# Kernel optimization log

Hardware: AMD Instinct MI355X
Metric: run time of the kernel (lower is better)

Reference implementation:

```python
import jax, jax.numpy as jnp
import numpy as np

D_MODEL = 1024
N_HEADS = 16
D_K = D_MODEL // N_HEADS
THETA = 10000.0
MAX_SEQ_LEN = 2048


def _rope_tables(seq_len):
    pos = jnp.arange(seq_len, dtype=jnp.float32)
    inv_freq = 1.0 / (THETA ** (jnp.arange(0, D_K, 2, dtype=jnp.float32) / D_K))
    ang = pos[:, None] * inv_freq[None, :]  # [T, D_K/2]
    return jnp.cos(ang), jnp.sin(ang)


def _apply_rope(x, cos, sin):
    # x: [..., T, D_K]; cos/sin: [T, D_K/2]
    x_even = x[..., ::2]
    x_odd = x[..., 1::2]
    r_even = x_even * cos - x_odd * sin
    r_odd = x_even * sin + x_odd * cos
    out = jnp.stack([r_even, r_odd], axis=-1)  # [..., T, D_K/2, 2]
    return out.reshape(x.shape)


def setup_inputs() -> dict:
    key = jax.random.key(0)
    ks = jax.random.split(key, 5)
    std = np.sqrt(2.0 / (D_MODEL + D_MODEL))
    x = jax.random.normal(ks[0], (2, 2048, D_MODEL), dtype=jnp.float32)
    w_q = jax.random.normal(ks[1], (D_MODEL, D_MODEL), dtype=jnp.float32) * std
    w_k = jax.random.normal(ks[2], (D_MODEL, D_MODEL), dtype=jnp.float32) * std
    w_v = jax.random.normal(ks[3], (D_MODEL, D_MODEL), dtype=jnp.float32) * std
    w_o = jax.random.normal(ks[4], (D_MODEL, D_MODEL), dtype=jnp.float32) * std
    return {"x": x, "w_q": w_q, "w_k": w_k, "w_v": w_v, "w_o": w_o}


def reference(x, w_q, w_k, w_v, w_o):
    B, T, _ = x.shape
    # projections: weight stored as [d_out, d_in], y = x @ W^T
    q = jnp.einsum('btd,od->bto', x, w_q)
    k = jnp.einsum('btd,od->bto', x, w_k)
    v = jnp.einsum('btd,od->bto', x, w_v)
    # split heads: [B, T, H*Dk] -> [B, H, T, Dk]
    q = q.reshape(B, T, N_HEADS, D_K).transpose(0, 2, 1, 3)
    k = k.reshape(B, T, N_HEADS, D_K).transpose(0, 2, 1, 3)
    v = v.reshape(B, T, N_HEADS, D_K).transpose(0, 2, 1, 3)
    cos, sin = _rope_tables(T)
    q = _apply_rope(q, cos, sin)
    k = _apply_rope(k, cos, sin)
    scores = jnp.einsum('bhqd,bhkd->bhqk', q, k) / np.sqrt(D_K).astype(np.float32)
    causal = jnp.tril(jnp.ones((T, T), dtype=bool))
    scores = jnp.where(causal, scores, -jnp.inf)
    attn = jax.nn.softmax(scores, axis=-1)
    out = jnp.einsum('bhqk,bhkd->bhqd', attn, v)
    out = out.transpose(0, 2, 1, 3).reshape(B, T, D_MODEL)
    return jnp.einsum('btd,od->bto', out, w_o)
```

## Files before the change

kernel.cpp:

```cpp
#include <hip/hip_runtime.h>
#include <hip/hip_bf16.h>

typedef __bf16 bf16_t;
typedef __bf16 bf16x8 __attribute__((ext_vector_type(8)));
typedef float f32x4 __attribute__((ext_vector_type(4)));
typedef short short4v __attribute__((ext_vector_type(4)));

#define D_MODEL 1024
#define T_SEQ 2048
#define NH 16
#define DKD 64
#define X_ELEMS (4194304u)
#define W_ELEMS (1048576u)

__device__ __forceinline__ void async16(const bf16_t* g, bf16_t* l) {
    __builtin_amdgcn_global_load_lds((const __attribute__((address_space(1))) void*)g,
                                     (__attribute__((address_space(3))) void*)l, 16, 0, 0);
}

__global__ __launch_bounds__(256) void convert_kernel(
    const float* __restrict__ x, const float* __restrict__ wq,
    const float* __restrict__ wk, const float* __restrict__ wv,
    const float* __restrict__ wo,
    bf16_t* __restrict__ xb, bf16_t* __restrict__ wqb, bf16_t* __restrict__ wkb,
    bf16_t* __restrict__ wvb, bf16_t* __restrict__ wob)
{
    size_t idx = ((size_t)blockIdx.x * 256 + threadIdx.x) * 4;
    const float* src; bf16_t* dst; size_t off;
    if (idx < X_ELEMS) { src = x; dst = xb; off = idx; }
    else {
        size_t r = idx - X_ELEMS;
        unsigned w = (unsigned)(r >> 20);
        off = r & (W_ELEMS - 1);
        src = (w == 0) ? wq : (w == 1) ? wk : (w == 2) ? wv : wo;
        dst = (w == 0) ? wqb : (w == 1) ? wkb : (w == 2) ? wvb : wob;
    }
    float4 v = *(const float4*)(src + off);
    union { bf16_t b[4]; short4v s; } u;
    u.b[0] = (bf16_t)v.x; u.b[1] = (bf16_t)v.y;
    u.b[2] = (bf16_t)v.z; u.b[3] = (bf16_t)v.w;
    *(short4v*)(dst + off) = u.s;
}

__global__ __launch_bounds__(256) void rope_kernel(float* __restrict__ cost, float* __restrict__ sint)
{
    int idx = blockIdx.x * 256 + threadIdx.x;
    int t = idx >> 5, i = idx & 31;
    float inv = expf(-0.28782313662425572f * (float)i);
    float ang = (float)t * inv;
    float s, c;
    sincosf(ang, &s, &c);
    cost[idx] = c; sint[idx] = s;
}

__global__ __launch_bounds__(256) void gemm_fused(
    const bf16_t* __restrict__ A,
    const bf16_t* __restrict__ W0, const bf16_t* __restrict__ W1, const bf16_t* __restrict__ W2,
    bf16_t* __restrict__ qout, bf16_t* __restrict__ kout, bf16_t* __restrict__ vout,
    const float* __restrict__ cost, const float* __restrict__ sint,
    float* __restrict__ fout, int modeBase)
{
    const int K = 1024;
    __shared__ bf16_t As[128 * 32];
    __shared__ bf16_t Bs[128 * 32];
    const int tid = threadIdx.x;
    const int wave = tid >> 6, lane = tid & 63;
    const int quad = lane >> 4, l16 = lane & 15;
    const int m0 = blockIdx.x * 128;
    const int n0 = blockIdx.y * 128;
    const int wm = (wave >> 1) * 64, wn = (wave & 1) * 64;
    const int mode = modeBase + blockIdx.z;
    const bf16_t* W = (mode == 1) ? W1 : (mode == 2) ? W2 : W0;

    const bf16_t* Afrag = (mode == 2) ? Bs : As;
    const bf16_t* Bfrag = (mode == 2) ? As : Bs;
    const int aoff = (mode == 2) ? wn : wm;
    const int boff = (mode == 2) ? wm : wn;

    const f32x4 fzero = {0.f, 0.f, 0.f, 0.f};
    f32x4 acc[4][4];
    #pragma unroll
    for (int i = 0; i < 4; ++i)
        #pragma unroll
        for (int j = 0; j < 4; ++j) acc[i][j] = fzero;

    for (int k0 = 0; k0 < K; k0 += 32) {
        __syncthreads();
        #pragma unroll
        for (int c = 0; c < 2; ++c) {
            int G = c * 256 + tid;
            int row = G >> 2, go = G & 3;
            async16(A + (size_t)(m0 + row) * K + (k0 + go * 8), As + (size_t)(c * 256 + wave * 64) * 8);
            async16(W + (size_t)(n0 + row) * K + (k0 + go * 8), Bs + (size_t)(c * 256 + wave * 64) * 8);
        }
        __syncthreads();
        bf16x8 af[4], bfv[4];
        #pragma unroll
        for (int mi = 0; mi < 4; ++mi)
            af[mi] = *(const bf16x8*)(Afrag + (aoff + mi * 16 + l16) * 32 + quad * 8);
        #pragma unroll
        for (int ni = 0; ni < 4; ++ni)
            bfv[ni] = *(const bf16x8*)(Bfrag + (boff + ni * 16 + l16) * 32 + quad * 8);
        #pragma unroll
        for (int mi = 0; mi < 4; ++mi)
            #pragma unroll
            for (int ni = 0; ni < 4; ++ni)
                acc[mi][ni] = __builtin_amdgcn_mfma_f32_16x16x32_bf16(af[mi], bfv[ni], acc[mi][ni], 0, 0, 0);
    }

    #pragma unroll
    for (int mi = 0; mi < 4; ++mi) {
        #pragma unroll
        for (int ni = 0; ni < 4; ++ni) {
            #pragma unroll
            for (int reg = 0; reg < 4; ++reg) {
                float v = acc[mi][ni][reg];
                if (mode == 2) {
                    int f   = n0 + wn + mi * 16 + quad * 4 + reg;
                    int tok = m0 + wm + ni * 16 + l16;
                    int t = tok & (T_SEQ - 1), b = tok >> 11;
                    int h = f >> 6, dk = f & 63;
                    vout[(((size_t)b * NH + h) * DKD + dk) * T_SEQ + t] = (bf16_t)v;
                } else {
                    int row = m0 + wm + mi * 16 + quad * 4 + reg;
                    int col = n0 + wn + ni * 16 + l16;
                    if (mode == 3) {
                        fout[(size_t)row * D_MODEL + col] = v;
                    } else {
                        int t = row & (T_SEQ - 1), b = row >> 11;
                        int h = col >> 6, dk = col & 63;
                        float vp = __shfl_xor(v, 1);
                        int fi = dk >> 1;
                        float c = cost[t * 32 + fi], s = sint[t * 32 + fi];
                        float r = (dk & 1) ? (vp * s + v * c) : (v * c - vp * s);
                        bf16_t* dst = (mode == 0) ? qout : kout;
                        dst[(((size_t)b * NH + h) * T_SEQ + t) * DKD + dk] = (bf16_t)r;
                    }
                }
            }
        }
    }
}

__global__ __launch_bounds__(256, 2) void attn_kernel(
    const bf16_t* __restrict__ Q, const bf16_t* __restrict__ Kb,
    const bf16_t* __restrict__ Vt, bf16_t* __restrict__ O)
{
    __shared__ bf16_t Ks[2][64 * 64];
    __shared__ bf16_t Vs[2][64 * 64];
    __shared__ bf16_t Pw[4][16 * 72];
    const int tid = threadIdx.x;
    const int wave = tid >> 6, lane = tid & 63;
    const int quad = lane >> 4, l16 = lane & 15;
    const int qb = (int)(gridDim.x - 1) - (int)blockIdx.x;
    const int bh = blockIdx.y;
    const int qw = qb * 128 + wave * 32;

    const bf16_t* kbase = Kb + (size_t)bh * T_SEQ * DKD;
    const bf16_t* vbase = Vt + (size_t)bh * DKD * T_SEQ;

    bf16x8 qf[2][2];
    #pragma unroll
    for (int j = 0; j < 2; ++j) {
        const bf16_t* qp = Q + ((size_t)bh * T_SEQ + qw + j * 16 + l16) * DKD;
        qf[j][0] = *(const bf16x8*)(qp + quad * 8);
        qf[j][1] = *(const bf16x8*)(qp + 32 + quad * 8);
    }
    const f32x4 fzero = {0.f, 0.f, 0.f, 0.f};
    f32x4 oacc[2][4];
    #pragma unroll
    for (int j = 0; j < 2; ++j)
        #pragma unroll
        for (int i = 0; i < 4; ++i) oacc[j][i] = fzero;
    float mrun[2] = {-__builtin_inff(), -__builtin_inff()};
    float lrun[2] = {0.f, 0.f};

    bf16_t* pw = &Pw[wave][0];
    const int nkt = 2 * qb + 2;

    auto stage = [&](int kt, int buf) {
        const int k0 = kt * 64;
        #pragma unroll
        for (int c = 0; c < 2; ++c) {
            int G = c * 256 + tid;
            int row = G >> 3, p = G & 7;
            int go = p ^ (row & 7);
            async16(kbase + (size_t)(k0 + row) * DKD + go * 8,
                    &Ks[buf][0] + (size_t)(c * 256 + wave * 64) * 8);
            async16(vbase + (size_t)row * T_SEQ + k0 + go * 8,
                    &Vs[buf][0] + (size_t)(c * 256 + wave * 64) * 8);
        }
    };

    stage(0, 0);
    for (int kt = 0; kt < nkt; ++kt) {
        __syncthreads();
        if (kt + 1 < nkt) stage(kt + 1, (kt + 1) & 1);
        const int k0 = kt * 64;
        if (k0 > qw + 31) continue;
        const bf16_t* Kc = &Ks[kt & 1][0];
        const bf16_t* Vc = &Vs[kt & 1][0];

        bf16x8 kf[4][2], vf[4][2];
        #pragma unroll
        for (int fi = 0; fi < 4; ++fi) {
            int r = fi * 16 + l16;
            #pragma unroll
            for (int ks = 0; ks < 2; ++ks) {
                int p = (ks * 4 + quad) ^ (r & 7);
                kf[fi][ks] = *(const bf16x8*)(Kc + r * 64 + p * 8);
                vf[fi][ks] = *(const bf16x8*)(Vc + r * 64 + p * 8);
            }
        }

        #pragma unroll
        for (int j = 0; j < 2; ++j) {
            const int qcol = qw + j * 16 + l16;
            if (k0 > qw + j * 16 + 15) continue;

            f32x4 s[4];
            #pragma unroll
            for (int fi = 0; fi < 4; ++fi) {
                f32x4 z = fzero;
                z = __builtin_amdgcn_mfma_f32_16x16x32_bf16(kf[fi][0], qf[j][0], z, 0, 0, 0);
                z = __builtin_amdgcn_mfma_f32_16x16x32_bf16(kf[fi][1], qf[j][1], z, 0, 0, 0);
                s[fi] = z;
            }
            float tm = -__builtin_inff();
            #pragma unroll
            for (int fi = 0; fi < 4; ++fi) {
                #pragma unroll
                for (int reg = 0; reg < 4; ++reg) {
                    float v = s[fi][reg] * 0.125f;
                    int key = k0 + fi * 16 + quad * 4 + reg;
                    v = (key > qcol) ? -__builtin_inff() : v;
                    s[fi][reg] = v;
                    tm = fmaxf(tm, v);
                }
            }
            tm = fmaxf(tm, __shfl_xor(tm, 16));
            tm = fmaxf(tm, __shfl_xor(tm, 32));
            float mnew = fmaxf(mrun[j], tm);
            float alpha = __expf(mrun[j] - mnew);
            mrun[j] = mnew;
            float sm = 0.f;
            #pragma unroll
            for (int fi = 0; fi < 4; ++fi) {
                #pragma unroll
                for (int reg = 0; reg < 4; ++reg) {
                    float p = __expf(s[fi][reg] - mnew);
                    s[fi][reg] = p;
                    sm += p;
                }
            }
            sm += __shfl_xor(sm, 16);
            sm += __shfl_xor(sm, 32);
            lrun[j] = lrun[j] * alpha + sm;
            #pragma unroll
            for (int di = 0; di < 4; ++di)
                #pragma unroll
                for (int reg = 0; reg < 4; ++reg) oacc[j][di][reg] *= alpha;

            #pragma unroll
            for (int fi = 0; fi < 4; ++fi) {
                union { bf16_t h[4]; unsigned long long u64; } pk;
                pk.h[0] = (bf16_t)s[fi][0]; pk.h[1] = (bf16_t)s[fi][1];
                pk.h[2] = (bf16_t)s[fi][2]; pk.h[3] = (bf16_t)s[fi][3];
                *(unsigned long long*)(pw + l16 * 72 + fi * 16 + quad * 4) = pk.u64;
            }
            bf16x8 pf[2];
            pf[0] = *(const bf16x8*)(pw + l16 * 72 + quad * 8);
            pf[1] = *(const bf16x8*)(pw + l16 * 72 + 32 + quad * 8);

            #pragma unroll
            for (int di = 0; di < 4; ++di) {
                oacc[j][di] = __builtin_amdgcn_mfma_f32_16x16x32_bf16(vf[di][0], pf[0], oacc[j][di], 0, 0, 0);
                oacc[j][di] = __builtin_amdgcn_mfma_f32_16x16x32_bf16(vf[di][1], pf[1], oacc[j][di], 0, 0, 0);
            }
        }
    }

    const int b = bh >> 4, h = bh & 15;
    #pragma unroll
    for (int j = 0; j < 2; ++j) {
        float rl = 1.0f / lrun[j];
        int q = qw + j * 16 + l16;
        #pragma unroll
        for (int di = 0; di < 4; ++di) {
            union { bf16_t hh[4]; unsigned long long u64; } ok;
            #pragma unroll
            for (int reg = 0; reg < 4; ++reg) ok.hh[reg] = (bf16_t)(oacc[j][di][reg] * rl);
            int d = di * 16 + quad * 4;
            *(unsigned long long*)(O + ((size_t)b * T_SEQ + q) * D_MODEL + h * DKD + d) = ok.u64;
        }
    }
}

extern "C" void kernel_launch(void* const* d_in, const int* in_sizes, int n_in,
                              void* d_out, int out_size, void* d_ws, size_t ws_size,
                              hipStream_t stream)
{
    const float* x  = (const float*)d_in[0];
    const float* wq = (const float*)d_in[1];
    const float* wk = (const float*)d_in[2];
    const float* wv = (const float*)d_in[3];
    const float* wo = (const float*)d_in[4];
    float* out = (float*)d_out;

    char* ws = (char*)d_ws;
    size_t off = 0;
    auto alloc = [&](size_t bytes) -> void* {
        void* p = ws + off; off += (bytes + 255) & ~(size_t)255; return p;
    };
    bf16_t* xb   = (bf16_t*)alloc((size_t)X_ELEMS * 2);
    bf16_t* wqb  = (bf16_t*)alloc((size_t)W_ELEMS * 2);
    bf16_t* wkb  = (bf16_t*)alloc((size_t)W_ELEMS * 2);
    bf16_t* wvb  = (bf16_t*)alloc((size_t)W_ELEMS * 2);
    bf16_t* wob  = (bf16_t*)alloc((size_t)W_ELEMS * 2);
    bf16_t* qb   = (bf16_t*)alloc((size_t)X_ELEMS * 2);
    bf16_t* kb   = (bf16_t*)alloc((size_t)X_ELEMS * 2);
    bf16_t* vtb  = (bf16_t*)alloc((size_t)X_ELEMS * 2);
    bf16_t* ob   = (bf16_t*)alloc((size_t)X_ELEMS * 2);
    float*  cost = (float*)alloc((size_t)T_SEQ * 32 * 4);
    float*  sint = (float*)alloc((size_t)T_SEQ * 32 * 4);

    convert_kernel<<<8192, 256, 0, stream>>>(x, wq, wk, wv, wo, xb, wqb, wkb, wvb, wob);
    rope_kernel<<<256, 256, 0, stream>>>(cost, sint);
    gemm_fused<<<dim3(32, 8, 3), 256, 0, stream>>>(xb, wqb, wkb, wvb, qb, kb, vtb, cost, sint, nullptr, 0);
    attn_kernel<<<dim3(16, 32), 256, 0, stream>>>(qb, kb, vtb, ob);
    gemm_fused<<<dim3(32, 8, 1), 256, 0, stream>>>(ob, wob, nullptr, nullptr, nullptr, nullptr, nullptr,
                                                   cost, sint, out, 3);
}
```

Measured before the change: 222.3 us.

## Restructure attention to single-wave blocks with register-prefetched K/V and exp2 softmax

Attention blocks shrink from four waves sharing LDS-staged K/V tiles to one wave per block handling 32 queries. K/V are loaded straight from global memory into registers, with the next K tile prefetched. The grid grows to 2048 small blocks and the __syncthreads barriers go away. The 1/sqrt(dk)·log2(e) scale is folded into Q in the projection epilogue so softmax can use exp2, and the causal mask is applied only on diagonal tiles. In exchange, K/V reuse across waves through LDS is lost, so each wave re-reads K/V from global or L2, and register pressure rises.

```diff
diff --git a/kernel.cpp b/kernel.cpp
--- a/kernel.cpp
+++ b/kernel.cpp
@@ -12,6 +12,7 @@
 #define DKD 64
 #define X_ELEMS (4194304u)
 #define W_ELEMS (1048576u)
+#define Q_SCALE 0.18033688011112042f
 
 __device__ __forceinline__ void async16(const bf16_t* g, bf16_t* l) {
     __builtin_amdgcn_global_load_lds((const __attribute__((address_space(1))) void*)g,
@@ -133,6 +134,7 @@
                         int fi = dk >> 1;
                         float c = cost[t * 32 + fi], s = sint[t * 32 + fi];
                         float r = (dk & 1) ? (vp * s + v * c) : (v * c - vp * s);
+                        if (mode == 0) r *= Q_SCALE;
                         bf16_t* dst = (mode == 0) ? qout : kout;
                         dst[(((size_t)b * NH + h) * T_SEQ + t) * DKD + dk] = (bf16_t)r;
                     }
@@ -142,19 +144,15 @@
     }
 }
 
-__global__ __launch_bounds__(256, 2) void attn_kernel(
+__global__ __launch_bounds__(64, 2) void attn_kernel(
     const bf16_t* __restrict__ Q, const bf16_t* __restrict__ Kb,
     const bf16_t* __restrict__ Vt, bf16_t* __restrict__ O)
 {
-    __shared__ bf16_t Ks[2][64 * 64];
-    __shared__ bf16_t Vs[2][64 * 64];
-    __shared__ bf16_t Pw[4][16 * 72];
-    const int tid = threadIdx.x;
-    const int wave = tid >> 6, lane = tid & 63;
+    __shared__ bf16_t Pw[2][16 * 72];
+    const int lane = threadIdx.x;
     const int quad = lane >> 4, l16 = lane & 15;
-    const int qb = (int)(gridDim.x - 1) - (int)blockIdx.x;
-    const int bh = blockIdx.y;
-    const int qw = qb * 128 + wave * 32;
+    const int bh = blockIdx.x;
+    const int qw = (63 - (int)blockIdx.y) * 32;
 
     const bf16_t* kbase = Kb + (size_t)bh * T_SEQ * DKD;
     const bf16_t* vbase = Vt + (size_t)bh * DKD * T_SEQ;
@@ -175,84 +173,76 @@
     float mrun[2] = {-__builtin_inff(), -__builtin_inff()};
     float lrun[2] = {0.f, 0.f};
 
-    bf16_t* pw = &Pw[wave][0];
-    const int nkt = 2 * qb + 2;
-
-    auto stage = [&](int kt, int buf) {
+    const int nkt = (qw + 95) >> 6;
+
+    bf16x8 kcur[4][2], knxt[4][2], vcur[4][2];
+    #pragma unroll
+    for (int fi = 0; fi < 4; ++fi) {
+        const bf16_t* kr = kbase + (size_t)(fi * 16 + l16) * DKD + quad * 8;
+        kcur[fi][0] = *(const bf16x8*)(kr);
+        kcur[fi][1] = *(const bf16x8*)(kr + 32);
+    }
+
+    for (int kt = 0; kt < nkt; ++kt) {
         const int k0 = kt * 64;
         #pragma unroll
-        for (int c = 0; c < 2; ++c) {
-            int G = c * 256 + tid;
-            int row = G >> 3, p = G & 7;
-            int go = p ^ (row & 7);
-            async16(kbase + (size_t)(k0 + row) * DKD + go * 8,
-                    &Ks[buf][0] + (size_t)(c * 256 + wave * 64) * 8);
-            async16(vbase + (size_t)row * T_SEQ + k0 + go * 8,
-                    &Vs[buf][0] + (size_t)(c * 256 + wave * 64) * 8);
-        }
-    };
-
-    stage(0, 0);
-    for (int kt = 0; kt < nkt; ++kt) {
-        __syncthreads();
-        if (kt + 1 < nkt) stage(kt + 1, (kt + 1) & 1);
-        const int k0 = kt * 64;
-        if (k0 > qw + 31) continue;
-        const bf16_t* Kc = &Ks[kt & 1][0];
-        const bf16_t* Vc = &Vs[kt & 1][0];
-
-        bf16x8 kf[4][2], vf[4][2];
-        #pragma unroll
-        for (int fi = 0; fi < 4; ++fi) {
-            int r = fi * 16 + l16;
-            #pragma unroll
-            for (int ks = 0; ks < 2; ++ks) {
-                int p = (ks * 4 + quad) ^ (r & 7);
-                kf[fi][ks] = *(const bf16x8*)(Kc + r * 64 + p * 8);
-                vf[fi][ks] = *(const bf16x8*)(Vc + r * 64 + p * 8);
+        for (int di = 0; di < 4; ++di) {
+            const bf16_t* vr = vbase + (size_t)(di * 16 + l16) * T_SEQ + k0 + quad * 8;
+            vcur[di][0] = *(const bf16x8*)(vr);
+            vcur[di][1] = *(const bf16x8*)(vr + 32);
+        }
+        if (kt + 1 < nkt) {
+            #pragma unroll
+            for (int fi = 0; fi < 4; ++fi) {
+                const bf16_t* kr = kbase + (size_t)(k0 + 64 + fi * 16 + l16) * DKD + quad * 8;
+                knxt[fi][0] = *(const bf16x8*)(kr);
+                knxt[fi][1] = *(const bf16x8*)(kr + 32);
             }
         }
 
         #pragma unroll
         for (int j = 0; j < 2; ++j) {
             const int qcol = qw + j * 16 + l16;
-            if (k0 > qw + j * 16 + 15) continue;
-
             f32x4 s[4];
             #pragma unroll
             for (int fi = 0; fi < 4; ++fi) {
                 f32x4 z = fzero;
-                z = __builtin_amdgcn_mfma_f32_16x16x32_bf16(kf[fi][0], qf[j][0], z, 0, 0, 0);
-                z = __builtin_amdgcn_mfma_f32_16x16x32_bf16(kf[fi][1], qf[j][1], z, 0, 0, 0);
+                z = __builtin_amdgcn_mfma_f32_16x16x32_bf16(kcur[fi][0], qf[j][0], z, 0, 0, 0);
+                z = __builtin_amdgcn_mfma_f32_16x16x32_bf16(kcur[fi][1], qf[j][1], z, 0, 0, 0);
                 s[fi] = z;
             }
             float tm = -__builtin_inff();
-            #pragma unroll
-            for (int fi = 0; fi < 4; ++fi) {
+            if (k0 + 63 > qw + j * 16) {
                 #pragma unroll
-                for (int reg = 0; reg < 4; ++reg) {
-                    float v = s[fi][reg] * 0.125f;
-                    int key = k0 + fi * 16 + quad * 4 + reg;
-                    v = (key > qcol) ? -__builtin_inff() : v;
-                    s[fi][reg] = v;
-                    tm = fmaxf(tm, v);
-                }
+                for (int fi = 0; fi < 4; ++fi)
+                    #pragma unroll
+                    for (int reg = 0; reg < 4; ++reg) {
+                        float v = s[fi][reg];
+                        int key = k0 + fi * 16 + quad * 4 + reg;
+                        v = (key > qcol) ? -__builtin_inff() : v;
+                        s[fi][reg] = v;
+                        tm = fmaxf(tm, v);
+                    }
+            } else {
+                #pragma unroll
+                for (int fi = 0; fi < 4; ++fi)
+                    #pragma unroll
+                    for (int reg = 0; reg < 4; ++reg) tm = fmaxf(tm, s[fi][reg]);
             }
             tm = fmaxf(tm, __shfl_xor(tm, 16));
             tm = fmaxf(tm, __shfl_xor(tm, 32));
             float mnew = fmaxf(mrun[j], tm);
-            float alpha = __expf(mrun[j] - mnew);
+            float alpha = __builtin_amdgcn_exp2f(mrun[j] - mnew);
             mrun[j] = mnew;
             float sm = 0.f;
             #pragma unroll
-            for (int fi = 0; fi < 4; ++fi) {
+            for (int fi = 0; fi < 4; ++fi)
                 #pragma unroll
                 for (int reg = 0; reg < 4; ++reg) {
-                    float p = __expf(s[fi][reg] - mnew);
+                    float p = __builtin_amdgcn_exp2f(s[fi][reg] - mnew);
                     s[fi][reg] = p;
                     sm += p;
                 }
-            }
             sm += __shfl_xor(sm, 16);
             sm += __shfl_xor(sm, 32);
             lrun[j] = lrun[j] * alpha + sm;
@@ -261,6 +251,7 @@
                 #pragma unroll
                 for (int reg = 0; reg < 4; ++reg) oacc[j][di][reg] *= alpha;
 
+            bf16_t* pw = &Pw[j][0];
             #pragma unroll
             for (int fi = 0; fi < 4; ++fi) {
                 union { bf16_t h[4]; unsigned long long u64; } pk;
@@ -274,8 +265,16 @@
 
             #pragma unroll
             for (int di = 0; di < 4; ++di) {
-                oacc[j][di] = __builtin_amdgcn_mfma_f32_16x16x32_bf16(vf[di][0], pf[0], oacc[j][di], 0, 0, 0);
-                oacc[j][di] = __builtin_amdgcn_mfma_f32_16x16x32_bf16(vf[di][1], pf[1], oacc[j][di], 0, 0, 0);
+                oacc[j][di] = __builtin_amdgcn_mfma_f32_16x16x32_bf16(vcur[di][0], pf[0], oacc[j][di], 0, 0, 0);
+                oacc[j][di] = __builtin_amdgcn_mfma_f32_16x16x32_bf16(vcur[di][1], pf[1], oacc[j][di], 0, 0, 0);
+            }
+        }
+
+        if (kt + 1 < nkt) {
+            #pragma unroll
+            for (int fi = 0; fi < 4; ++fi) {
+                kcur[fi][0] = knxt[fi][0];
+                kcur[fi][1] = knxt[fi][1];
             }
         }
     }
@@ -327,7 +326,7 @@
     convert_kernel<<<8192, 256, 0, stream>>>(x, wq, wk, wv, wo, xb, wqb, wkb, wvb, wob);
     rope_kernel<<<256, 256, 0, stream>>>(cost, sint);
     gemm_fused<<<dim3(32, 8, 3), 256, 0, stream>>>(xb, wqb, wkb, wvb, qb, kb, vtb, cost, sint, nullptr, 0);
-    attn_kernel<<<dim3(16, 32), 256, 0, stream>>>(qb, kb, vtb, ob);
+    attn_kernel<<<dim3(32, 64), 64, 0, stream>>>(qb, kb, vtb, ob);
     gemm_fused<<<dim3(32, 8, 1), 256, 0, stream>>>(ob, wob, nullptr, nullptr, nullptr, nullptr, nullptr,
                                                    cost, sint, out, 3);
 }
```

New measurement: 222.7 us. Within noise of the previous version (+0.2%).
